# Optimization experiments

Hardware: AMD Instinct MI355X
Metric: run time of the kernel (lower is better)

Reference implementation:

```python
import jax, jax.numpy as jnp
import numpy as np

B, T, C, H = 128, 256, 512, 2048
STEP_SIZE = 0.001
TOTAL = 1.0 / (T - 1)                       # uniform linspace(0,1,T) interval length
STEPS_HINT = max(1, int(TOTAL / STEP_SIZE))
N_SUB = max(1, int(max(STEPS_HINT, TOTAL / STEP_SIZE)))  # = 3 fixed RK4 substeps per interval
DT = TOTAL / N_SUB


def setup_inputs() -> dict:
    key = jax.random.key(0)
    ks = jax.random.split(key, 7)
    def lin_w(k, fi, fo):
        return (jax.random.uniform(k, (fi, fo), jnp.float32, -1.0, 1.0) / np.sqrt(fi)).astype(jnp.float32)
    def lin_b(k, fi, fo):
        return (jax.random.uniform(k, (fo,), jnp.float32, -1.0, 1.0) / np.sqrt(fi)).astype(jnp.float32)
    x = jax.random.normal(ks[0], (B, T, C), jnp.float32)
    return {
        "x": x,
        "W1": lin_w(ks[1], C, H), "b1": lin_b(ks[2], C, H),
        "W2": lin_w(ks[3], H, H), "b2": lin_b(ks[4], H, H),
        "W3": lin_w(ks[5], H, C), "b3": lin_b(ks[6], H, C),
    }


def _mlp(y, W1, b1, W2, b2, W3, b3):
    # f(y) = Linear(Tanh(Linear(Tanh(Linear(y)))))
    h = jnp.tanh(y @ W1 + b1)
    h = jnp.tanh(h @ W2 + b2)
    return h @ W3 + b3


def _rk4_step(y, dt, p):
    k1 = _mlp(y, *p)
    k2 = _mlp(y + 0.5 * dt * k1, *p)
    k3 = _mlp(y + 0.5 * dt * k2, *p)
    k4 = _mlp(y + dt * k3, *p)
    return y + (dt / 6.0) * (k1 + 2.0 * k2 + 2.0 * k3 + k4)


def reference(x, W1, b1, W2, b2, W3, b3):
    p = (W1, b1, W2, b2, W3, b3)
    def interval(y, _):
        for _ in range(N_SUB):  # static, small unroll (3)
            y = _rk4_step(y, DT, p)
        return y, y
    y0 = x[:, 0, :]                                   # [B, C]
    _, ys = jax.lax.scan(interval, y0, None, length=T - 1)  # ys: [T-1, B, C]
    return jnp.concatenate([x[:, :1, :], jnp.moveaxis(ys, 0, 1)], axis=1)  # [B, T, C]
```

## Files before the change

kernel.cpp:

```cpp
#include <hip/hip_runtime.h>
#include <hip/hip_bf16.h>
#include <cstdint>

#define B_ 128
#define T_ 256
#define C_ 512
#define H_ 2048
#define NWG 256
#define NTHR 256
#define NGROUP 8
#define GSIZE 32
#define M_ 16
#define FSTRIDE 16
#define RSU 134
#define RSS 536
#define DT_F 0.0013071895424836601f

typedef __bf16 bf16x8 __attribute__((ext_vector_type(8)));
typedef short s16x8 __attribute__((ext_vector_type(8)));
typedef float f32x4 __attribute__((ext_vector_type(4)));
typedef unsigned long long ull;

enum : size_t {
  OFF_FLAGS = 0,
  OFF_W1P = 32768,
  OFF_W2P = OFF_W1P + (size_t)C_ * H_ * 2,
  OFF_W3P = OFF_W2P + (size_t)H_ * H_ * 2,
  OFF_U   = OFF_W3P + (size_t)H_ * C_ * 2,
  OFF_H1  = OFF_U   + (size_t)NGROUP * M_ * C_ * 2,
  OFF_H2  = OFF_H1  + (size_t)NGROUP * M_ * H_ * 2,
  WS_END  = OFF_H2  + (size_t)NGROUP * M_ * H_ * 2
};

__device__ __forceinline__ bf16x8 ld_frag(const unsigned short* p) {
  s16x8 v = *reinterpret_cast<const s16x8*>(p);
  return __builtin_bit_cast(bf16x8, v);
}
__device__ __forceinline__ bf16x8 lds_frag(const unsigned short* p) {
  s16x8 v = *reinterpret_cast<const s16x8*>(p);
  return __builtin_bit_cast(bf16x8, v);
}
__device__ __forceinline__ void st_coh16(unsigned short* p, unsigned short v) {
  __hip_atomic_store(p, v, __ATOMIC_RELAXED, __HIP_MEMORY_SCOPE_AGENT);
}
__device__ __forceinline__ f32x4 mfma16(bf16x8 a, bf16x8 b, f32x4 c) {
  return __builtin_amdgcn_mfma_f32_16x16x32_bf16(a, b, c, 0, 0, 0);
}
__device__ __forceinline__ unsigned short tobf(float f) {
  return __builtin_bit_cast(unsigned short, (__bf16)f);
}
__device__ __forceinline__ float fast_tanh(float v) {
  float e = __expf(2.0f * v);
  return 1.0f - 2.0f / (e + 1.0f);
}

__global__ void init_flags_k(unsigned* f) {
  int i = blockIdx.x * 256 + threadIdx.x;
  if (i < NGROUP * GSIZE * FSTRIDE) f[i] = 0u;
}

__global__ void swizzle_w_k(const float* __restrict__ W, unsigned short* __restrict__ Wp,
                            int N, int kblog) {
  int idx = blockIdx.x * 256 + threadIdx.x;
  int j = idx & 7;
  int l = (idx >> 3) & 63;
  int rem = idx >> 9;
  int kb = rem & ((1 << kblog) - 1);
  int nt = rem >> kblog;
  int k = kb * 32 + ((l >> 4) << 3) + j;
  int n = (nt << 4) + (l & 15);
  Wp[idx] = tobf(W[(size_t)k * N + n]);
}

__device__ __forceinline__ void bar_arrive(unsigned* gf, int gn, unsigned gen) {
  asm volatile("s_waitcnt vmcnt(0)" ::: "memory");
  __syncthreads();
  if (threadIdx.x == 0)
    __hip_atomic_store(&gf[gn * FSTRIDE], gen, __ATOMIC_RELAXED, __HIP_MEMORY_SCOPE_AGENT);
}
__device__ __forceinline__ void bar_wait(unsigned* gf, unsigned gen) {
  if (threadIdx.x < GSIZE) {
    while (__hip_atomic_load(&gf[threadIdx.x * FSTRIDE], __ATOMIC_RELAXED,
                             __HIP_MEMORY_SCOPE_AGENT) < gen)
      __builtin_amdgcn_s_sleep(1);
  }
  __syncthreads();
}

__device__ __forceinline__ void issue_l1(const ull* __restrict__ g, int tid, ull v[8]) {
  #pragma unroll
  for (int j = 0; j < 8; ++j)
    v[j] = __hip_atomic_load(g + j * NTHR + tid, __ATOMIC_RELAXED, __HIP_MEMORY_SCOPE_AGENT);
}
__device__ __forceinline__ void issue_chunk(const ull* __restrict__ g, int tid, ull v[8]) {
  #pragma unroll
  for (int j = 0; j < 8; ++j) {
    int i = j * NTHR + tid;
    v[j] = __hip_atomic_load(g + (size_t)(i >> 7) * 512 + (i & 127),
                             __ATOMIC_RELAXED, __HIP_MEMORY_SCOPE_AGENT);
  }
}
__device__ __forceinline__ void commit(ull* __restrict__ lds, int tid, const ull v[8]) {
  #pragma unroll
  for (int j = 0; j < 8; ++j) {
    int i = j * NTHR + tid;
    lds[(i >> 7) * RSU + (i & 127)] = v[j];
  }
}

__global__ __launch_bounds__(NTHR, 1) void ode_persist_k(
    const float* __restrict__ x, const float* __restrict__ b1,
    const float* __restrict__ b2, const float* __restrict__ b3,
    float* __restrict__ out, unsigned char* __restrict__ ws) {
  const int wg = blockIdx.x, tid = threadIdx.x;
  const int g = wg >> 5, gn = wg & 31;
  const int wave = tid >> 6, lane = tid & 63;
  const int lhi = lane >> 4, llo = lane & 15;

  unsigned* gflags = (unsigned*)(ws + OFF_FLAGS) + g * GSIZE * FSTRIDE;
  const unsigned short* W1p = (const unsigned short*)(ws + OFF_W1P);
  const unsigned short* W2p = (const unsigned short*)(ws + OFF_W2P);
  const unsigned short* W3p = (const unsigned short*)(ws + OFF_W3P);
  const ull* ubuf_u = (const ull*)(ws + OFF_U)  + (size_t)g * (M_ * C_ / 4);
  const ull* h1_u   = (const ull*)(ws + OFF_H1) + (size_t)g * (M_ * H_ / 4);
  const ull* h2_u   = (const ull*)(ws + OFF_H2) + (size_t)g * (M_ * H_ / 4);
  unsigned short* ubuf_s = (unsigned short*)(ws + OFF_U)  + (size_t)g * M_ * C_;
  unsigned short* h1_s   = (unsigned short*)(ws + OFF_H1) + (size_t)g * M_ * H_;
  unsigned short* h2_s   = (unsigned short*)(ws + OFF_H2) + (size_t)g * M_ * H_;

  __shared__ alignas(16) ull atile[2][M_ * RSU];
  __shared__ float red[4][256];
  __shared__ float ytile[256], k1t[256], k2t[256], k3t[256];

  const int n16 = gn * 4 + wave;
  const unsigned short* bp1 = W1p + (size_t)n16 * 16 * 512 + lane * 8;
  const unsigned short* bp2 = W2p + (size_t)n16 * 64 * 512 + lane * 8;
  const unsigned short* bp3 = W3p + (size_t)gn  * 64 * 512 + lane * 8;

  bf16x8 w1r[16], w3r[16];
  #pragma unroll
  for (int kb = 0; kb < 16; ++kb) w1r[kb] = ld_frag(bp1 + kb * 512);
  #pragma unroll
  for (int q = 0; q < 16; ++q)
    w3r[q] = ld_frag(bp3 + ((q >> 2) * 16 + wave * 4 + (q & 3)) * 512);

  {
    int row = tid >> 4, c16 = tid & 15;
    int col = gn * 16 + c16;
    int b = g * M_ + row;
    float v = x[(size_t)b * (T_ * C_) + col];
    ytile[tid] = v;
    out[(size_t)b * (T_ * C_) + col] = v;
    st_coh16(&ubuf_s[row * C_ + col], tobf(v));
  }
  unsigned gen = 0;
  bar_arrive(gflags, gn, ++gen);
  bar_wait(gflags, gen);

  ull v[8];
  #pragma unroll 1
  for (int t = 0; t < T_ - 1; ++t) {
    #pragma unroll 1
    for (int sub = 0; sub < 3; ++sub) {
      #pragma unroll 1
      for (int st = 0; st < 4; ++st) {
        issue_l1(ubuf_u, tid, v);
        commit(atile[0], tid, v);
        __syncthreads();
        {
          f32x4 acc = {0.f, 0.f, 0.f, 0.f};
          const unsigned short* al = (const unsigned short*)atile[0] + llo * RSS + lhi * 8;
          #pragma unroll
          for (int kb = 0; kb < 16; ++kb)
            acc = mfma16(lds_frag(al + kb * 32), w1r[kb], acc);
          const int col = n16 * 16 + llo;
          const float bb = b1[col];
          #pragma unroll
          for (int r = 0; r < 4; ++r)
            st_coh16(&h1_s[(lhi * 4 + r) * H_ + col], tobf(fast_tanh(acc[r] + bb)));
        }
        bar_arrive(gflags, gn, ++gen);
        bf16x8 pf[8];
        #pragma unroll
        for (int q = 0; q < 8; ++q) pf[q] = ld_frag(bp2 + q * 512);
        bar_wait(gflags, gen);

        {
          f32x4 acc = {0.f, 0.f, 0.f, 0.f};
          issue_chunk(h1_u, tid, v);
          commit(atile[0], tid, v);
          __syncthreads();
          issue_chunk(h1_u + 128, tid, v);
          {
            const unsigned short* al = (const unsigned short*)atile[0] + llo * RSS + lhi * 8;
            #pragma unroll
            for (int kb = 0; kb < 8; ++kb)
              acc = mfma16(lds_frag(al + kb * 32), pf[kb], acc);
            #pragma unroll
            for (int kb = 8; kb < 16; ++kb)
              acc = mfma16(lds_frag(al + kb * 32), ld_frag(bp2 + kb * 512), acc);
          }
          commit(atile[1], tid, v);
          __syncthreads();
          #pragma unroll
          for (int c = 1; c < 4; ++c) {
            if (c < 3) issue_chunk(h1_u + (c + 1) * 128, tid, v);
            const unsigned short* al = (const unsigned short*)atile[c & 1] + llo * RSS + lhi * 8;
            #pragma unroll
            for (int kb = 0; kb < 16; ++kb)
              acc = mfma16(lds_frag(al + kb * 32), ld_frag(bp2 + (c * 16 + kb) * 512), acc);
            if (c < 3) commit(atile[(c + 1) & 1], tid, v);
            __syncthreads();
          }
          const int col = n16 * 16 + llo;
          const float bb = b2[col];
          #pragma unroll
          for (int r = 0; r < 4; ++r)
            st_coh16(&h2_s[(lhi * 4 + r) * H_ + col], tobf(fast_tanh(acc[r] + bb)));
        }
        bar_arrive(gflags, gn, ++gen);
        bar_wait(gflags, gen);

        {
          f32x4 acc = {0.f, 0.f, 0.f, 0.f};
          issue_chunk(h2_u, tid, v);
          commit(atile[0], tid, v);
          __syncthreads();
          #pragma unroll
          for (int c = 0; c < 4; ++c) {
            if (c < 3) issue_chunk(h2_u + (c + 1) * 128, tid, v);
            const unsigned short* al = (const unsigned short*)atile[c & 1] + llo * RSS + lhi * 8;
            #pragma unroll
            for (int jj = 0; jj < 4; ++jj)
              acc = mfma16(lds_frag(al + (wave * 4 + jj) * 32), w3r[c * 4 + jj], acc);
            if (c < 3) commit(atile[(c + 1) & 1], tid, v);
            __syncthreads();
          }
          #pragma unroll
          for (int r = 0; r < 4; ++r) red[wave][(lhi * 4 + r) * 16 + llo] = acc[r];
          __syncthreads();
          if (wave == 0) {
            const float dt = DT_F;
            const float bb = b3[gn * 16 + llo];
            #pragma unroll
            for (int r = 0; r < 4; ++r) {
              int row = lhi * 4 + r;
              int i = row * 16 + llo;
              float z = red[0][i] + red[1][i] + red[2][i] + red[3][i] + bb;
              float yv = ytile[i];
              unsigned short* up = &ubuf_s[row * C_ + gn * 16 + llo];
              if (st == 0)      { k1t[i] = z; st_coh16(up, tobf(yv + 0.5f * dt * z)); }
              else if (st == 1) { k2t[i] = z; st_coh16(up, tobf(yv + 0.5f * dt * z)); }
              else if (st == 2) { k3t[i] = z; st_coh16(up, tobf(yv + dt * z)); }
              else {
                float yn = yv + (dt * (1.0f / 6.0f)) * (k1t[i] + 2.f * k2t[i] + 2.f * k3t[i] + z);
                ytile[i] = yn;
                st_coh16(up, tobf(yn));
                if (sub == 2)
                  out[(size_t)(g * M_ + row) * (T_ * C_) + (size_t)(t + 1) * C_ + gn * 16 + llo] = yn;
              }
            }
          }
        }
        bar_arrive(gflags, gn, ++gen);
        bar_wait(gflags, gen);
      }
    }
  }
}

extern "C" void kernel_launch(void* const* d_in, const int* in_sizes, int n_in,
                              void* d_out, int out_size, void* d_ws, size_t ws_size,
                              hipStream_t stream) {
  (void)in_sizes; (void)n_in; (void)out_size; (void)ws_size;
  const float* x  = (const float*)d_in[0];
  const float* W1 = (const float*)d_in[1];
  const float* b1 = (const float*)d_in[2];
  const float* W2 = (const float*)d_in[3];
  const float* b2 = (const float*)d_in[4];
  const float* W3 = (const float*)d_in[5];
  const float* b3 = (const float*)d_in[6];
  float* out = (float*)d_out;
  unsigned char* ws = (unsigned char*)d_ws;

  init_flags_k<<<16, 256, 0, stream>>>((unsigned*)(ws + OFF_FLAGS));
  swizzle_w_k<<<(C_ * H_) / 256, 256, 0, stream>>>(W1, (unsigned short*)(ws + OFF_W1P), H_, 4);
  swizzle_w_k<<<(H_ * H_) / 256, 256, 0, stream>>>(W2, (unsigned short*)(ws + OFF_W2P), H_, 6);
  swizzle_w_k<<<(H_ * C_) / 256, 256, 0, stream>>>(W3, (unsigned short*)(ws + OFF_W3P), C_, 6);

  ode_persist_k<<<NWG, NTHR, 0, stream>>>(x, b1, b2, b3, out, ws);
}
```

Measured before the change: 51.85 ms.

## Keep W2 fragments register-resident, deepen LDS prefetch, split MFMA accumulators

The full per-wave W2 slice (64 bf16x8 fragments) now lives in registers instead of being streamed from global memory on every layer-2 pass. W1 fragments are loaded per step, with the loads overlapped with the U tile fetch. Layer-2 and layer-3 activation chunks use two register buffers so two chunks are in flight ahead of the MFMAs. Each GEMM uses two independent accumulators to break the MFMA dependency chain, the LDS row pad shrinks from 134 to 132, and the bias loads are hoisted out of the loop. This adds heavy VGPR pressure (about 256 extra registers for w2r) and risks spills, and the new padding may change LDS bank conflicts.

```diff
diff --git a/kernel.cpp b/kernel.cpp
--- a/kernel.cpp
+++ b/kernel.cpp
@@ -12,8 +12,8 @@
 #define GSIZE 32
 #define M_ 16
 #define FSTRIDE 16
-#define RSU 134
-#define RSS 536
+#define RSU1 132
+#define RSS1 528
 #define DT_F 0.0013071895424836601f
 
 typedef __bf16 bf16x8 __attribute__((ext_vector_type(8)));
@@ -87,12 +87,12 @@
   __syncthreads();
 }
 
-__device__ __forceinline__ void issue_l1(const ull* __restrict__ g, int tid, ull v[8]) {
+__device__ __forceinline__ void issue_u(const ull* __restrict__ g, int tid, ull v[8]) {
   #pragma unroll
   for (int j = 0; j < 8; ++j)
     v[j] = __hip_atomic_load(g + j * NTHR + tid, __ATOMIC_RELAXED, __HIP_MEMORY_SCOPE_AGENT);
 }
-__device__ __forceinline__ void issue_chunk(const ull* __restrict__ g, int tid, ull v[8]) {
+__device__ __forceinline__ void issue_c(const ull* __restrict__ g, int tid, ull v[8]) {
   #pragma unroll
   for (int j = 0; j < 8; ++j) {
     int i = j * NTHR + tid;
@@ -104,9 +104,25 @@
   #pragma unroll
   for (int j = 0; j < 8; ++j) {
     int i = j * NTHR + tid;
-    lds[(i >> 7) * RSU + (i & 127)] = v[j];
-  }
-}
+    lds[(i >> 7) * RSU1 + (i & 127)] = v[j];
+  }
+}
+
+#define L2CHUNK(c, buf) {                                                     \
+  const unsigned short* al = (const unsigned short*)atile[buf] + llo * RSS1 + lhi * 8; \
+  _Pragma("unroll")                                                           \
+  for (int jj = 0; jj < 8; ++jj) {                                            \
+    acc0 = mfma16(lds_frag(al + (2 * jj) * 32),     w2r[(c) * 16 + 2 * jj],     acc0); \
+    acc1 = mfma16(lds_frag(al + (2 * jj + 1) * 32), w2r[(c) * 16 + 2 * jj + 1], acc1); \
+  } }
+
+#define L3CHUNK(c, buf) {                                                     \
+  const unsigned short* al = (const unsigned short*)atile[buf] + llo * RSS1 + lhi * 8; \
+  _Pragma("unroll")                                                           \
+  for (int jj = 0; jj < 2; ++jj) {                                            \
+    acc0 = mfma16(lds_frag(al + (wave * 4 + 2 * jj) * 32),     w3r[(c) * 4 + 2 * jj],     acc0); \
+    acc1 = mfma16(lds_frag(al + (wave * 4 + 2 * jj + 1) * 32), w3r[(c) * 4 + 2 * jj + 1], acc1); \
+  } }
 
 __global__ __launch_bounds__(NTHR, 1) void ode_persist_k(
     const float* __restrict__ x, const float* __restrict__ b1,
@@ -128,7 +144,7 @@
   unsigned short* h1_s   = (unsigned short*)(ws + OFF_H1) + (size_t)g * M_ * H_;
   unsigned short* h2_s   = (unsigned short*)(ws + OFF_H2) + (size_t)g * M_ * H_;
 
-  __shared__ alignas(16) ull atile[2][M_ * RSU];
+  __shared__ alignas(16) ull atile[2][M_ * RSU1];
   __shared__ float red[4][256];
   __shared__ float ytile[256], k1t[256], k2t[256], k3t[256];
 
@@ -137,12 +153,16 @@
   const unsigned short* bp2 = W2p + (size_t)n16 * 64 * 512 + lane * 8;
   const unsigned short* bp3 = W3p + (size_t)gn  * 64 * 512 + lane * 8;
 
-  bf16x8 w1r[16], w3r[16];
-  #pragma unroll
-  for (int kb = 0; kb < 16; ++kb) w1r[kb] = ld_frag(bp1 + kb * 512);
+  bf16x8 w2r[64], w3r[16];
+  #pragma unroll
+  for (int kb = 0; kb < 64; ++kb) w2r[kb] = ld_frag(bp2 + kb * 512);
   #pragma unroll
   for (int q = 0; q < 16; ++q)
     w3r[q] = ld_frag(bp3 + ((q >> 2) * 16 + wave * 4 + (q & 3)) * 512);
+
+  const float bb1 = b1[n16 * 16 + llo];
+  const float bb2 = b2[n16 * 16 + llo];
+  const float bb3 = b3[gn * 16 + llo];
 
   {
     int row = tid >> 4, c16 = tid & 15;
@@ -157,96 +177,92 @@
   bar_arrive(gflags, gn, ++gen);
   bar_wait(gflags, gen);
 
-  ull v[8];
+  ull va[8], vb[8];
   #pragma unroll 1
   for (int t = 0; t < T_ - 1; ++t) {
     #pragma unroll 1
     for (int sub = 0; sub < 3; ++sub) {
       #pragma unroll 1
       for (int st = 0; st < 4; ++st) {
-        issue_l1(ubuf_u, tid, v);
-        commit(atile[0], tid, v);
-        __syncthreads();
         {
-          f32x4 acc = {0.f, 0.f, 0.f, 0.f};
-          const unsigned short* al = (const unsigned short*)atile[0] + llo * RSS + lhi * 8;
-          #pragma unroll
-          for (int kb = 0; kb < 16; ++kb)
-            acc = mfma16(lds_frag(al + kb * 32), w1r[kb], acc);
+          issue_u(ubuf_u, tid, va);
+          bf16x8 w1f[16];
+          #pragma unroll
+          for (int kb = 0; kb < 16; ++kb) w1f[kb] = ld_frag(bp1 + kb * 512);
+          commit(atile[0], tid, va);
+          __syncthreads();
+          f32x4 acc0 = {0.f, 0.f, 0.f, 0.f}, acc1 = {0.f, 0.f, 0.f, 0.f};
+          const unsigned short* al = (const unsigned short*)atile[0] + llo * RSS1 + lhi * 8;
+          #pragma unroll
+          for (int jj = 0; jj < 8; ++jj) {
+            acc0 = mfma16(lds_frag(al + (2 * jj) * 32),     w1f[2 * jj],     acc0);
+            acc1 = mfma16(lds_frag(al + (2 * jj + 1) * 32), w1f[2 * jj + 1], acc1);
+          }
+          f32x4 a = acc0 + acc1;
           const int col = n16 * 16 + llo;
-          const float bb = b1[col];
           #pragma unroll
           for (int r = 0; r < 4; ++r)
-            st_coh16(&h1_s[(lhi * 4 + r) * H_ + col], tobf(fast_tanh(acc[r] + bb)));
-        }
-        bar_arrive(gflags, gn, ++gen);
-        bf16x8 pf[8];
-        #pragma unroll
-        for (int q = 0; q < 8; ++q) pf[q] = ld_frag(bp2 + q * 512);
-        bar_wait(gflags, gen);
-
-        {
-          f32x4 acc = {0.f, 0.f, 0.f, 0.f};
-          issue_chunk(h1_u, tid, v);
-          commit(atile[0], tid, v);
-          __syncthreads();
-          issue_chunk(h1_u + 128, tid, v);
-          {
-            const unsigned short* al = (const unsigned short*)atile[0] + llo * RSS + lhi * 8;
-            #pragma unroll
-            for (int kb = 0; kb < 8; ++kb)
-              acc = mfma16(lds_frag(al + kb * 32), pf[kb], acc);
-            #pragma unroll
-            for (int kb = 8; kb < 16; ++kb)
-              acc = mfma16(lds_frag(al + kb * 32), ld_frag(bp2 + kb * 512), acc);
-          }
-          commit(atile[1], tid, v);
-          __syncthreads();
-          #pragma unroll
-          for (int c = 1; c < 4; ++c) {
-            if (c < 3) issue_chunk(h1_u + (c + 1) * 128, tid, v);
-            const unsigned short* al = (const unsigned short*)atile[c & 1] + llo * RSS + lhi * 8;
-            #pragma unroll
-            for (int kb = 0; kb < 16; ++kb)
-              acc = mfma16(lds_frag(al + kb * 32), ld_frag(bp2 + (c * 16 + kb) * 512), acc);
-            if (c < 3) commit(atile[(c + 1) & 1], tid, v);
-            __syncthreads();
-          }
-          const int col = n16 * 16 + llo;
-          const float bb = b2[col];
-          #pragma unroll
-          for (int r = 0; r < 4; ++r)
-            st_coh16(&h2_s[(lhi * 4 + r) * H_ + col], tobf(fast_tanh(acc[r] + bb)));
+            st_coh16(&h1_s[(lhi * 4 + r) * H_ + col], tobf(fast_tanh(a[r] + bb1)));
         }
         bar_arrive(gflags, gn, ++gen);
         bar_wait(gflags, gen);
 
         {
-          f32x4 acc = {0.f, 0.f, 0.f, 0.f};
-          issue_chunk(h2_u, tid, v);
-          commit(atile[0], tid, v);
-          __syncthreads();
-          #pragma unroll
-          for (int c = 0; c < 4; ++c) {
-            if (c < 3) issue_chunk(h2_u + (c + 1) * 128, tid, v);
-            const unsigned short* al = (const unsigned short*)atile[c & 1] + llo * RSS + lhi * 8;
-            #pragma unroll
-            for (int jj = 0; jj < 4; ++jj)
-              acc = mfma16(lds_frag(al + (wave * 4 + jj) * 32), w3r[c * 4 + jj], acc);
-            if (c < 3) commit(atile[(c + 1) & 1], tid, v);
-            __syncthreads();
-          }
-          #pragma unroll
-          for (int r = 0; r < 4; ++r) red[wave][(lhi * 4 + r) * 16 + llo] = acc[r];
+          f32x4 acc0 = {0.f, 0.f, 0.f, 0.f}, acc1 = {0.f, 0.f, 0.f, 0.f};
+          issue_c(h1_u,       tid, va);
+          issue_c(h1_u + 128, tid, vb);
+          commit(atile[0], tid, va);
+          __syncthreads();
+          issue_c(h1_u + 256, tid, va);
+          L2CHUNK(0, 0);
+          commit(atile[1], tid, vb);
+          __syncthreads();
+          issue_c(h1_u + 384, tid, vb);
+          L2CHUNK(1, 1);
+          commit(atile[0], tid, va);
+          __syncthreads();
+          L2CHUNK(2, 0);
+          commit(atile[1], tid, vb);
+          __syncthreads();
+          L2CHUNK(3, 1);
+          f32x4 a = acc0 + acc1;
+          const int col = n16 * 16 + llo;
+          #pragma unroll
+          for (int r = 0; r < 4; ++r)
+            st_coh16(&h2_s[(lhi * 4 + r) * H_ + col], tobf(fast_tanh(a[r] + bb2)));
+        }
+        bar_arrive(gflags, gn, ++gen);
+        bar_wait(gflags, gen);
+
+        {
+          f32x4 acc0 = {0.f, 0.f, 0.f, 0.f}, acc1 = {0.f, 0.f, 0.f, 0.f};
+          issue_c(h2_u,       tid, va);
+          issue_c(h2_u + 128, tid, vb);
+          commit(atile[0], tid, va);
+          __syncthreads();
+          issue_c(h2_u + 256, tid, va);
+          L3CHUNK(0, 0);
+          commit(atile[1], tid, vb);
+          __syncthreads();
+          issue_c(h2_u + 384, tid, vb);
+          L3CHUNK(1, 1);
+          commit(atile[0], tid, va);
+          __syncthreads();
+          L3CHUNK(2, 0);
+          commit(atile[1], tid, vb);
+          __syncthreads();
+          L3CHUNK(3, 1);
+          f32x4 a = acc0 + acc1;
+          #pragma unroll
+          for (int r = 0; r < 4; ++r) red[wave][(lhi * 4 + r) * 16 + llo] = a[r];
           __syncthreads();
           if (wave == 0) {
             const float dt = DT_F;
-            const float bb = b3[gn * 16 + llo];
             #pragma unroll
             for (int r = 0; r < 4; ++r) {
               int row = lhi * 4 + r;
               int i = row * 16 + llo;
-              float z = red[0][i] + red[1][i] + red[2][i] + red[3][i] + bb;
+              float z = red[0][i] + red[1][i] + red[2][i] + red[3][i] + bb3;
               float yv = ytile[i];
               unsigned short* up = &ubuf_s[row * C_ + gn * 16 + llo];
               if (st == 0)      { k1t[i] = z; st_coh16(up, tobf(yv + 0.5f * dt * z)); }
```

Measured after the change: 43.78 ms. -15.6%, faster.
